# Optimization experiments

Measured on AMD Instinct MI355X. Metric: run time of the kernel, lower is better.

The kernel has to match this reference:

```python
import jax, jax.numpy as jnp
import numpy as np

B, N, S, K = 8, 16384, 1024, 32
C_STEM, C_PATCH, PE_DIM = 64, 128, 24
RADIUS = 0.2
NUM_BANDS = PE_DIM // 6  # 4 freq bands, sin+cos per xyz axis -> 3*2*4 = 24


def setup_inputs() -> dict:
    key = jax.random.key(0)
    ks = jax.random.split(key, 6)
    xyz = jax.random.uniform(ks[0], (B, N, 3), dtype=jnp.float32)
    point_feature = jax.random.normal(ks[1], (B, N, C_STEM), dtype=jnp.float32)
    patch_center = jax.random.uniform(ks[2], (B, S, 3), dtype=jnp.float32)
    in_dim = C_STEM + 3 + PE_DIM  # grouped_feature + relative_xyz + pos-enc
    w1 = jax.random.normal(ks[3], (in_dim, C_PATCH), dtype=jnp.float32) / np.sqrt(in_dim)
    b1 = jnp.zeros((C_PATCH,), dtype=jnp.float32)
    w2 = jax.random.normal(ks[4], (C_PATCH, C_PATCH), dtype=jnp.float32) / np.sqrt(C_PATCH)
    b2 = jnp.zeros((C_PATCH,), dtype=jnp.float32)
    return dict(xyz=xyz, point_feature=point_feature, patch_center=patch_center,
                w1=w1, b1=b1, w2=w2, b2=b2)


def query_ball_point(radius, nsample, xyz, new_xyz):
    # Standard PointNet++ ball query. xyz:[B,N,3], new_xyz:[B,S,3] -> idx:[B,S,K]
    n = xyz.shape[1]
    sqrdists = jnp.sum((new_xyz[:, :, None, :] - xyz[:, None, :, :]) ** 2, axis=-1)  # [B,S,N]
    gi = jnp.where(sqrdists > radius * radius, n,
                   jnp.arange(n, dtype=jnp.int32)[None, None, :])
    gi = jnp.sort(gi, axis=-1)[:, :, :nsample]           # first K in-ball indices
    first = gi[:, :, :1]
    gi = jnp.where(gi == n, first, gi)                   # pad misses with first hit
    return jnp.minimum(gi, n - 1)


def index_points(points, idx):
    # points:[B,N,C], idx:[B,S,K] -> [B,S,K,C]
    b = points.shape[0]
    return points[jnp.arange(b)[:, None, None], idx]


def pos_encode(rel):
    # NeRF-style sinusoidal encoding of relative xyz: [...,3] -> [...,PE_DIM]
    freqs = (2.0 ** jnp.arange(NUM_BANDS, dtype=jnp.float32)) * jnp.pi
    ang = rel[..., None] * freqs                          # [...,3,NB]
    enc = jnp.concatenate([jnp.sin(ang), jnp.cos(ang)], axis=-1)  # [...,3,2NB]
    return enc.reshape(rel.shape[:-1] + (PE_DIM,))


def reference(xyz, point_feature, patch_center, w1, b1, w2, b2):
    neighbor_idx = query_ball_point(RADIUS, K, xyz, patch_center)   # [B,S,K]
    grouped_xyz = index_points(xyz, neighbor_idx)                    # [B,S,K,3]
    grouped_feature = index_points(point_feature, neighbor_idx)      # [B,S,K,C_STEM]
    relative_xyz = grouped_xyz - patch_center[:, :, None, :]
    relative_position = pos_encode(relative_xyz)                     # [B,S,K,PE_DIM]
    grouped_input = jnp.concatenate(
        (grouped_feature, relative_xyz, relative_position), axis=-1)  # [B,S,K,91]
    h = jax.nn.relu(grouped_input @ w1 + b1)   # PointMLP 1 (shared per-point MLP)
    h = h @ w2 + b2                            # PointMLP 2 (no activation)
    patch_feature = jnp.max(h, axis=2)         # max-pool over K neighbors -> [B,S,C_PATCH]
    return (patch_feature, neighbor_idx)
```

## Files before the change

### kernel.cpp

```cpp
#include <hip/hip_runtime.h>
#include <hip/hip_bf16.h>

#define B_ 8
#define N_ 16384
#define S_ 1024
#define K_ 32
#define CSTEM 64
#define CPATCH 128
#define INDIM 91
#define LDH 136

typedef __attribute__((ext_vector_type(8))) short short8v;
typedef __attribute__((ext_vector_type(4))) float f32x4;

static __device__ __forceinline__ unsigned short f2bf(float f) {
  union { float f; unsigned int u; } v; v.f = f;
  return (unsigned short)((v.u + 0x7FFFu + ((v.u >> 16) & 1u)) >> 16);
}

static __device__ __forceinline__ short8v cvt8(const float4 a, const float4 b) {
  unsigned short v[8];
  v[0] = f2bf(a.x); v[1] = f2bf(a.y); v[2] = f2bf(a.z); v[3] = f2bf(a.w);
  v[4] = f2bf(b.x); v[5] = f2bf(b.y); v[6] = f2bf(b.z); v[7] = f2bf(b.w);
  return *(const short8v*)v;
}

static __device__ __forceinline__ short8v pe_frag(
    float r0, float r1, float r2, int kq)
{
  unsigned short v[8];
  #pragma unroll
  for (int j = 0; j < 8; ++j) {
    const int c = 64 + kq + j;
    float val;
    if (c < 67) {
      val = (c == 64) ? r0 : ((c == 65) ? r1 : r2);
    } else if (c < 91) {
      const int qq = c - 67, d = qq >> 3, rbit = qq & 7, band = rbit & 3;
      const float rel = (d == 0) ? r0 : ((d == 1) ? r1 : r2);
      const float ang = rel * ((float)(1 << band) * 3.14159265358979323846f);
      val = (rbit < 4) ? __sinf(ang) : __cosf(ang);
    } else {
      val = 0.f;
    }
    v[j] = f2bf(val);
  }
  return *(const short8v*)v;
}

__global__ __launch_bounds__(256) void pack_weights(
    const float* __restrict__ w1, const float* __restrict__ w2,
    unsigned short* __restrict__ w1p, unsigned short* __restrict__ w2p)
{
  const int id = blockIdx.x * 256 + threadIdx.x;
  if (id < 3 * 8 * 64) {
    const int l = id & 63, ct = (id >> 6) & 7, ks = id >> 9;
    const int col = 16 * ct + (l & 15);
    const int kb = 32 * ks + (l >> 4) * 8;
    unsigned short v[8];
    #pragma unroll
    for (int j = 0; j < 8; ++j) {
      const int k = kb + j;
      v[j] = (k < INDIM) ? f2bf(w1[k * CPATCH + col]) : (unsigned short)0;
    }
    *(short8v*)&w1p[(size_t)id * 8] = *(const short8v*)v;
  } else if (id < 3 * 8 * 64 + 4 * 8 * 64) {
    const int id2 = id - 3 * 8 * 64;
    const int l = id2 & 63, ct = (id2 >> 6) & 7, ks = id2 >> 9;
    const int col = 16 * ct + (l & 15);
    const int kb = 32 * ks + (l >> 4) * 8;
    unsigned short v[8];
    #pragma unroll
    for (int j = 0; j < 8; ++j) v[j] = f2bf(w2[(kb + j) * CPATCH + col]);
    *(short8v*)&w2p[(size_t)id2 * 8] = *(const short8v*)v;
  }
}

#define TEST4(V0, V1, V2, MASKVAR) do {                                    \
    MASKVAR = 0u;                                                          \
    const float X[4] = {(V0).x, (V0).w, (V1).z, (V2).y};                   \
    const float Y[4] = {(V0).y, (V1).x, (V1).w, (V2).z};                   \
    const float Z[4] = {(V0).z, (V1).y, (V2).x, (V2).w};                   \
    _Pragma("unroll")                                                      \
    for (int p = 0; p < 4; ++p) {                                          \
      const float dxf = X[p] - cx, dyf = Y[p] - cy, dzf = Z[p] - cz;       \
      const float d2f = fmaf(dxf, dxf, fmaf(dyf, dyf, dzf * dzf));         \
      bool in;                                                             \
      if (fabsf(d2f - 0.04f) <= 1e-5f) {                                   \
        const double dx = (double)X[p] - (double)cx;                       \
        const double dy = (double)Y[p] - (double)cy;                       \
        const double dz = (double)Z[p] - (double)cz;                       \
        in = (dx * dx + dy * dy + dz * dz) <= (0.2 * 0.2);                 \
      } else {                                                             \
        in = (d2f < 0.04f);                                                \
      }                                                                    \
      if (in) MASKVAR |= (1u << p);                                        \
    }                                                                      \
  } while (0)

#define APPEND4(MASKVAR, POSVAR, I0, V0, V1, V2) do {                      \
    if ((MASKVAR) & 1u) { if ((POSVAR) < K_) { sidx[POSVAR] = (I0) + 0;    \
      sxyz[POSVAR][0] = (V0).x; sxyz[POSVAR][1] = (V0).y;                  \
      sxyz[POSVAR][2] = (V0).z; } ++(POSVAR); }                            \
    if ((MASKVAR) & 2u) { if ((POSVAR) < K_) { sidx[POSVAR] = (I0) + 1;    \
      sxyz[POSVAR][0] = (V0).w; sxyz[POSVAR][1] = (V1).x;                  \
      sxyz[POSVAR][2] = (V1).y; } ++(POSVAR); }                            \
    if ((MASKVAR) & 4u) { if ((POSVAR) < K_) { sidx[POSVAR] = (I0) + 2;    \
      sxyz[POSVAR][0] = (V1).z; sxyz[POSVAR][1] = (V1).w;                  \
      sxyz[POSVAR][2] = (V2).x; } ++(POSVAR); }                            \
    if ((MASKVAR) & 8u) { if ((POSVAR) < K_) { sidx[POSVAR] = (I0) + 3;    \
      sxyz[POSVAR][0] = (V2).y; sxyz[POSVAR][1] = (V2).z;                  \
      sxyz[POSVAR][2] = (V2).w; } ++(POSVAR); }                            \
  } while (0)

__global__ __launch_bounds__(64, 4) void fused_wave(
    const float* __restrict__ xyz, const float* __restrict__ pf,
    const float* __restrict__ pc,
    const unsigned short* __restrict__ w1p, const float* __restrict__ b1,
    const unsigned short* __restrict__ w2p, const float* __restrict__ b2,
    float* __restrict__ idx_out, float* __restrict__ out)
{
  const int lane = threadIdx.x;
  const int bs   = blockIdx.x;
  const int b    = bs >> 10;

  __shared__ int   sidx[K_];
  __shared__ float sxyz[K_][3];
  __shared__ __align__(16) unsigned short Hs[K_][LDH];

  const float* __restrict__ xb  = xyz + (size_t)b * N_ * 3;
  const float* __restrict__ pfb = pf  + (size_t)b * N_ * CSTEM;
  const float cx = pc[bs * 3 + 0];
  const float cy = pc[bs * 3 + 1];
  const float cz = pc[bs * 3 + 2];

  int found = 0;
  {
    const int lo3 = lane * 12;
    int base = 0;
    float4 v0 = *(const float4*)&xb[lo3 + 0];
    float4 v1 = *(const float4*)&xb[lo3 + 4];
    float4 v2 = *(const float4*)&xb[lo3 + 8];
    float4 v3 = *(const float4*)&xb[256 * 3 + lo3 + 0];
    float4 v4 = *(const float4*)&xb[256 * 3 + lo3 + 4];
    float4 v5 = *(const float4*)&xb[256 * 3 + lo3 + 8];

    for (;;) {
      const int nb = (base + 512 < N_) ? base + 512 : base;
      const float4 n0 = *(const float4*)&xb[nb * 3 + lo3 + 0];
      const float4 n1 = *(const float4*)&xb[nb * 3 + lo3 + 4];
      const float4 n2 = *(const float4*)&xb[nb * 3 + lo3 + 8];
      const float4 n3 = *(const float4*)&xb[(nb + 256) * 3 + lo3 + 0];
      const float4 n4 = *(const float4*)&xb[(nb + 256) * 3 + lo3 + 4];
      const float4 n5 = *(const float4*)&xb[(nb + 256) * 3 + lo3 + 8];

      unsigned m0, m1;
      TEST4(v0, v1, v2, m0);
      TEST4(v3, v4, v5, m1);

      const int c0 = __popc(m0), c1 = __popc(m1);
      unsigned incl = (unsigned)c0 | ((unsigned)c1 << 16);
      #pragma unroll
      for (int d = 1; d < 64; d <<= 1) {
        const unsigned t = (unsigned)__shfl_up((int)incl, d);
        if (lane >= d) incl += t;
      }
      const unsigned tot = (unsigned)__shfl((int)incl, 63);
      const int t0 = (int)(tot & 0xFFFFu), t1 = (int)(tot >> 16);

      int pos0 = found + (int)((incl & 0xFFFFu)) - c0;
      int pos1 = found + t0 + (int)(incl >> 16) - c1;
      const int i0 = base + lane * 4;
      APPEND4(m0, pos0, i0, v0, v1, v2);
      APPEND4(m1, pos1, i0 + 256, v3, v4, v5);

      found += t0 + t1;
      if (found >= K_) break;
      base += 512;
      if (base >= N_) break;
      v0 = n0; v1 = n1; v2 = n2; v3 = n3; v4 = n4; v5 = n5;
    }
  }

  if (lane == 0 && found == 0) {
    sidx[0] = N_ - 1;
    sxyz[0][0] = xb[(N_ - 1) * 3 + 0];
    sxyz[0][1] = xb[(N_ - 1) * 3 + 1];
    sxyz[0][2] = xb[(N_ - 1) * 3 + 2];
  }
  __threadfence_block();

  if (lane < K_) {
    const int   fill = sidx[0];
    const float fx = sxyz[0][0];
    const float fy = sxyz[0][1];
    const float fz = sxyz[0][2];
    const int v = (lane < found) ? sidx[lane] : fill;
    if (lane >= found) {
      sidx[lane] = fill;
      sxyz[lane][0] = fx;
      sxyz[lane][1] = fy;
      sxyz[lane][2] = fz;
    }
    idx_out[(size_t)bs * K_ + lane] = (float)v;
  }
  __threadfence_block();

  const int rfr  = lane & 15;
  const int koff = (lane >> 4) * 8;

  const int r0 = sidx[rfr];
  const int r1 = sidx[16 + rfr];
  const float4 u00 = *(const float4*)&pfb[(size_t)r0 * CSTEM + koff];
  const float4 u01 = *(const float4*)&pfb[(size_t)r0 * CSTEM + koff + 4];
  const float4 u02 = *(const float4*)&pfb[(size_t)r0 * CSTEM + 32 + koff];
  const float4 u03 = *(const float4*)&pfb[(size_t)r0 * CSTEM + 32 + koff + 4];
  const float4 u10 = *(const float4*)&pfb[(size_t)r1 * CSTEM + koff];
  const float4 u11 = *(const float4*)&pfb[(size_t)r1 * CSTEM + koff + 4];
  const float4 u12 = *(const float4*)&pfb[(size_t)r1 * CSTEM + 32 + koff];
  const float4 u13 = *(const float4*)&pfb[(size_t)r1 * CSTEM + 32 + koff + 4];

  const short8v a0k2 = pe_frag(sxyz[rfr][0] - cx,
                               sxyz[rfr][1] - cy,
                               sxyz[rfr][2] - cz, koff);
  const short8v a1k2 = pe_frag(sxyz[16 + rfr][0] - cx,
                               sxyz[16 + rfr][1] - cy,
                               sxyz[16 + rfr][2] - cz, koff);
  const short8v a0k0 = cvt8(u00, u01), a0k1 = cvt8(u02, u03);
  const short8v a1k0 = cvt8(u10, u11), a1k1 = cvt8(u12, u13);

  #pragma unroll
  for (int c = 0; c < 4; ++c) {
    const short8v bA0 = *(const short8v*)&w1p[((size_t)(0 * 8 + 2 * c + 0) * 64 + lane) * 8];
    const short8v bA1 = *(const short8v*)&w1p[((size_t)(0 * 8 + 2 * c + 1) * 64 + lane) * 8];
    const short8v bB0 = *(const short8v*)&w1p[((size_t)(1 * 8 + 2 * c + 0) * 64 + lane) * 8];
    const short8v bB1 = *(const short8v*)&w1p[((size_t)(1 * 8 + 2 * c + 1) * 64 + lane) * 8];
    const short8v bC0 = *(const short8v*)&w1p[((size_t)(2 * 8 + 2 * c + 0) * 64 + lane) * 8];
    const short8v bC1 = *(const short8v*)&w1p[((size_t)(2 * 8 + 2 * c + 1) * 64 + lane) * 8];

    f32x4 acc[2][2] = {};
    acc[0][0] = __builtin_amdgcn_mfma_f32_16x16x32_bf16(a0k0, bA0, acc[0][0], 0, 0, 0);
    acc[0][1] = __builtin_amdgcn_mfma_f32_16x16x32_bf16(a0k0, bA1, acc[0][1], 0, 0, 0);
    acc[1][0] = __builtin_amdgcn_mfma_f32_16x16x32_bf16(a1k0, bA0, acc[1][0], 0, 0, 0);
    acc[1][1] = __builtin_amdgcn_mfma_f32_16x16x32_bf16(a1k0, bA1, acc[1][1], 0, 0, 0);
    acc[0][0] = __builtin_amdgcn_mfma_f32_16x16x32_bf16(a0k1, bB0, acc[0][0], 0, 0, 0);
    acc[0][1] = __builtin_amdgcn_mfma_f32_16x16x32_bf16(a0k1, bB1, acc[0][1], 0, 0, 0);
    acc[1][0] = __builtin_amdgcn_mfma_f32_16x16x32_bf16(a1k1, bB0, acc[1][0], 0, 0, 0);
    acc[1][1] = __builtin_amdgcn_mfma_f32_16x16x32_bf16(a1k1, bB1, acc[1][1], 0, 0, 0);
    acc[0][0] = __builtin_amdgcn_mfma_f32_16x16x32_bf16(a0k2, bC0, acc[0][0], 0, 0, 0);
    acc[0][1] = __builtin_amdgcn_mfma_f32_16x16x32_bf16(a0k2, bC1, acc[0][1], 0, 0, 0);
    acc[1][0] = __builtin_amdgcn_mfma_f32_16x16x32_bf16(a1k2, bC0, acc[1][0], 0, 0, 0);
    acc[1][1] = __builtin_amdgcn_mfma_f32_16x16x32_bf16(a1k2, bC1, acc[1][1], 0, 0, 0);

    const float bia0 = b1[32 * c + rfr];
    const float bia1 = b1[32 * c + 16 + rfr];
    #pragma unroll
    for (int rt = 0; rt < 2; ++rt)
      #pragma unroll
      for (int reg = 0; reg < 4; ++reg) {
        const int row = 16 * rt + (lane >> 4) * 4 + reg;
        Hs[row][32 * c + rfr]      = f2bf(fmaxf(acc[rt][0][reg] + bia0, 0.f));
        Hs[row][32 * c + 16 + rfr] = f2bf(fmaxf(acc[rt][1][reg] + bia1, 0.f));
      }
  }

  short8v hf[8];
  #pragma unroll
  for (int ks = 0; ks < 4; ++ks) {
    hf[ks * 2 + 0] = *(const short8v*)&Hs[rfr][ks * 32 + koff];
    hf[ks * 2 + 1] = *(const short8v*)&Hs[16 + rfr][ks * 32 + koff];
  }

  #pragma unroll
  for (int c = 0; c < 4; ++c) {
    f32x4 acc2[2][2] = {};
    #pragma unroll
    for (int ks = 0; ks < 4; ++ks) {
      const short8v b0 = *(const short8v*)&w2p[((size_t)(ks * 8 + 2 * c + 0) * 64 + lane) * 8];
      const short8v b1v = *(const short8v*)&w2p[((size_t)(ks * 8 + 2 * c + 1) * 64 + lane) * 8];
      acc2[0][0] = __builtin_amdgcn_mfma_f32_16x16x32_bf16(hf[ks * 2 + 0], b0,  acc2[0][0], 0, 0, 0);
      acc2[0][1] = __builtin_amdgcn_mfma_f32_16x16x32_bf16(hf[ks * 2 + 0], b1v, acc2[0][1], 0, 0, 0);
      acc2[1][0] = __builtin_amdgcn_mfma_f32_16x16x32_bf16(hf[ks * 2 + 1], b0,  acc2[1][0], 0, 0, 0);
      acc2[1][1] = __builtin_amdgcn_mfma_f32_16x16x32_bf16(hf[ks * 2 + 1], b1v, acc2[1][1], 0, 0, 0);
    }
    float m0 = -3.4e38f, m1 = -3.4e38f;
    #pragma unroll
    for (int rt = 0; rt < 2; ++rt)
      #pragma unroll
      for (int reg = 0; reg < 4; ++reg) {
        m0 = fmaxf(m0, acc2[rt][0][reg]);
        m1 = fmaxf(m1, acc2[rt][1][reg]);
      }
    m0 += b2[32 * c + rfr];
    m1 += b2[32 * c + 16 + rfr];
    m0 = fmaxf(m0, __shfl_xor(m0, 16));
    m0 = fmaxf(m0, __shfl_xor(m0, 32));
    m1 = fmaxf(m1, __shfl_xor(m1, 16));
    m1 = fmaxf(m1, __shfl_xor(m1, 32));
    if (lane < 16) {
      out[(size_t)bs * CPATCH + 32 * c + lane]      = m0;
      out[(size_t)bs * CPATCH + 32 * c + 16 + lane] = m1;
    }
  }
}

extern "C" void kernel_launch(void* const* d_in, const int* in_sizes, int n_in,
                              void* d_out, int out_size, void* d_ws, size_t ws_size,
                              hipStream_t stream) {
  const float* xyz = (const float*)d_in[0];
  const float* pf  = (const float*)d_in[1];
  const float* pc  = (const float*)d_in[2];
  const float* w1  = (const float*)d_in[3];
  const float* b1  = (const float*)d_in[4];
  const float* w2  = (const float*)d_in[5];
  const float* b2  = (const float*)d_in[6];

  float* out     = (float*)d_out;
  float* idx_out = out + (size_t)B_ * S_ * CPATCH;

  unsigned short* w1p = (unsigned short*)d_ws;
  unsigned short* w2p = w1p + 96 * 128;

  pack_weights<<<14, 256, 0, stream>>>(w1, w2, w1p, w2p);
  fused_wave<<<B_ * S_, 64, 0, stream>>>(xyz, pf, pc, w1p, b1, w2p, b2,
                                         idx_out, out);
}
```

Baseline: 46.60 us.

## Hoist fp64 ball-boundary fix out of hot loop and software-pipeline weight loads

The ball-query test now computes an in-mask and a near-boundary band mask in fp32, and runs the fp64 recheck only when some lane in the wave has a band hit. That keeps the double-precision branch out of the common path. The padding pass that rewrote shared sidx/sxyz behind a second fence is removed; consumers select entry 0 for slots beyond `found`. The W1 and W2 fragment loads are double-buffered so the next chunk's weights are fetched while the current MFMAs run, at the cost of more live vector registers.

```diff
diff --git a/kernel.cpp b/kernel.cpp
--- a/kernel.cpp
+++ b/kernel.cpp
@@ -76,8 +76,8 @@
   }
 }
 
-#define TEST4(V0, V1, V2, MASKVAR) do {                                    \
-    MASKVAR = 0u;                                                          \
+#define TEST4FB(V0, V1, V2, MASKVAR, BANDVAR) do {                         \
+    MASKVAR = 0u; BANDVAR = 0u;                                            \
     const float X[4] = {(V0).x, (V0).w, (V1).z, (V2).y};                   \
     const float Y[4] = {(V0).y, (V1).x, (V1).w, (V2).z};                   \
     const float Z[4] = {(V0).z, (V1).y, (V2).x, (V2).w};                   \
@@ -85,16 +85,26 @@
     for (int p = 0; p < 4; ++p) {                                          \
       const float dxf = X[p] - cx, dyf = Y[p] - cy, dzf = Z[p] - cz;       \
       const float d2f = fmaf(dxf, dxf, fmaf(dyf, dyf, dzf * dzf));         \
-      bool in;                                                             \
-      if (fabsf(d2f - 0.04f) <= 1e-5f) {                                   \
-        const double dx = (double)X[p] - (double)cx;                       \
-        const double dy = (double)Y[p] - (double)cy;                       \
-        const double dz = (double)Z[p] - (double)cz;                       \
-        in = (dx * dx + dy * dy + dz * dz) <= (0.2 * 0.2);                 \
-      } else {                                                             \
-        in = (d2f < 0.04f);                                                \
+      if (fabsf(d2f - 0.04f) <= 1e-5f) BANDVAR |= (1u << p);               \
+      if (d2f < 0.04f) MASKVAR |= (1u << p);                               \
+    }                                                                      \
+  } while (0)
+
+#define FIX4(BANDVAR, MASKVAR, V0, V1, V2) do {                            \
+    if (BANDVAR) {                                                         \
+      const float X[4] = {(V0).x, (V0).w, (V1).z, (V2).y};                 \
+      const float Y[4] = {(V0).y, (V1).x, (V1).w, (V2).z};                 \
+      const float Z[4] = {(V0).z, (V1).y, (V2).x, (V2).w};                 \
+      _Pragma("unroll")                                                    \
+      for (int p = 0; p < 4; ++p) {                                        \
+        if ((BANDVAR >> p) & 1u) {                                         \
+          const double dx = (double)X[p] - (double)cx;                     \
+          const double dy = (double)Y[p] - (double)cy;                     \
+          const double dz = (double)Z[p] - (double)cz;                     \
+          const bool in64 = (dx * dx + dy * dy + dz * dz) <= (0.2 * 0.2);  \
+          MASKVAR = (MASKVAR & ~(1u << p)) | ((unsigned)in64 << p);        \
+        }                                                                  \
       }                                                                    \
-      if (in) MASKVAR |= (1u << p);                                        \
     }                                                                      \
   } while (0)
 
@@ -113,6 +123,11 @@
       sxyz[POSVAR][2] = (V2).w; } ++(POSVAR); }                            \
   } while (0)
 
+#define LDW1(KS, C, T) \
+  (*(const short8v*)&w1p[((size_t)((KS) * 8 + 2 * (C) + (T)) * 64 + lane) * 8])
+#define LDW2(KS, C, T) \
+  (*(const short8v*)&w2p[((size_t)((KS) * 8 + 2 * (C) + (T)) * 64 + lane) * 8])
+
 __global__ __launch_bounds__(64, 4) void fused_wave(
     const float* __restrict__ xyz, const float* __restrict__ pf,
     const float* __restrict__ pc,
@@ -154,9 +169,13 @@
       const float4 n4 = *(const float4*)&xb[(nb + 256) * 3 + lo3 + 4];
       const float4 n5 = *(const float4*)&xb[(nb + 256) * 3 + lo3 + 8];
 
-      unsigned m0, m1;
-      TEST4(v0, v1, v2, m0);
-      TEST4(v3, v4, v5, m1);
+      unsigned m0, m1, bd0, bd1;
+      TEST4FB(v0, v1, v2, m0, bd0);
+      TEST4FB(v3, v4, v5, m1, bd1);
+      if (__any((int)(bd0 | bd1))) {
+        FIX4(bd0, m0, v0, v1, v2);
+        FIX4(bd1, m1, v3, v4, v5);
+      }
 
       const int c0 = __popc(m0), c1 = __popc(m1);
       unsigned incl = (unsigned)c0 | ((unsigned)c1 << 16);
@@ -168,7 +187,7 @@
       const unsigned tot = (unsigned)__shfl((int)incl, 63);
       const int t0 = (int)(tot & 0xFFFFu), t1 = (int)(tot >> 16);
 
-      int pos0 = found + (int)((incl & 0xFFFFu)) - c0;
+      int pos0 = found + (int)(incl & 0xFFFFu) - c0;
       int pos1 = found + t0 + (int)(incl >> 16) - c1;
       const int i0 = base + lane * 4;
       APPEND4(m0, pos0, i0, v0, v1, v2);
@@ -190,27 +209,12 @@
   }
   __threadfence_block();
 
-  if (lane < K_) {
-    const int   fill = sidx[0];
-    const float fx = sxyz[0][0];
-    const float fy = sxyz[0][1];
-    const float fz = sxyz[0][2];
-    const int v = (lane < found) ? sidx[lane] : fill;
-    if (lane >= found) {
-      sidx[lane] = fill;
-      sxyz[lane][0] = fx;
-      sxyz[lane][1] = fy;
-      sxyz[lane][2] = fz;
-    }
-    idx_out[(size_t)bs * K_ + lane] = (float)v;
-  }
-  __threadfence_block();
-
   const int rfr  = lane & 15;
   const int koff = (lane >> 4) * 8;
 
-  const int r0 = sidx[rfr];
-  const int r1 = sidx[16 + rfr];
+  const int r0 = (rfr < found)      ? sidx[rfr]      : sidx[0];
+  const int r1 = (16 + rfr < found) ? sidx[16 + rfr] : sidx[0];
+
   const float4 u00 = *(const float4*)&pfb[(size_t)r0 * CSTEM + koff];
   const float4 u01 = *(const float4*)&pfb[(size_t)r0 * CSTEM + koff + 4];
   const float4 u02 = *(const float4*)&pfb[(size_t)r0 * CSTEM + 32 + koff];
@@ -220,49 +224,66 @@
   const float4 u12 = *(const float4*)&pfb[(size_t)r1 * CSTEM + 32 + koff];
   const float4 u13 = *(const float4*)&pfb[(size_t)r1 * CSTEM + 32 + koff + 4];
 
-  const short8v a0k2 = pe_frag(sxyz[rfr][0] - cx,
-                               sxyz[rfr][1] - cy,
-                               sxyz[rfr][2] - cz, koff);
-  const short8v a1k2 = pe_frag(sxyz[16 + rfr][0] - cx,
-                               sxyz[16 + rfr][1] - cy,
-                               sxyz[16 + rfr][2] - cz, koff);
+  if (lane < K_) {
+    const int vout = (lane < found) ? sidx[lane] : sidx[0];
+    idx_out[(size_t)bs * K_ + lane] = (float)vout;
+  }
+
+  const float sxa = (rfr < found) ? sxyz[rfr][0] : sxyz[0][0];
+  const float sya = (rfr < found) ? sxyz[rfr][1] : sxyz[0][1];
+  const float sza = (rfr < found) ? sxyz[rfr][2] : sxyz[0][2];
+  const float sxb2 = (16 + rfr < found) ? sxyz[16 + rfr][0] : sxyz[0][0];
+  const float syb2 = (16 + rfr < found) ? sxyz[16 + rfr][1] : sxyz[0][1];
+  const float szb2 = (16 + rfr < found) ? sxyz[16 + rfr][2] : sxyz[0][2];
+
+  const short8v a0k2 = pe_frag(sxa - cx, sya - cy, sza - cz, koff);
+  const short8v a1k2 = pe_frag(sxb2 - cx, syb2 - cy, szb2 - cz, koff);
   const short8v a0k0 = cvt8(u00, u01), a0k1 = cvt8(u02, u03);
   const short8v a1k0 = cvt8(u10, u11), a1k1 = cvt8(u12, u13);
 
-  #pragma unroll
-  for (int c = 0; c < 4; ++c) {
-    const short8v bA0 = *(const short8v*)&w1p[((size_t)(0 * 8 + 2 * c + 0) * 64 + lane) * 8];
-    const short8v bA1 = *(const short8v*)&w1p[((size_t)(0 * 8 + 2 * c + 1) * 64 + lane) * 8];
-    const short8v bB0 = *(const short8v*)&w1p[((size_t)(1 * 8 + 2 * c + 0) * 64 + lane) * 8];
-    const short8v bB1 = *(const short8v*)&w1p[((size_t)(1 * 8 + 2 * c + 1) * 64 + lane) * 8];
-    const short8v bC0 = *(const short8v*)&w1p[((size_t)(2 * 8 + 2 * c + 0) * 64 + lane) * 8];
-    const short8v bC1 = *(const short8v*)&w1p[((size_t)(2 * 8 + 2 * c + 1) * 64 + lane) * 8];
-
-    f32x4 acc[2][2] = {};
-    acc[0][0] = __builtin_amdgcn_mfma_f32_16x16x32_bf16(a0k0, bA0, acc[0][0], 0, 0, 0);
-    acc[0][1] = __builtin_amdgcn_mfma_f32_16x16x32_bf16(a0k0, bA1, acc[0][1], 0, 0, 0);
-    acc[1][0] = __builtin_amdgcn_mfma_f32_16x16x32_bf16(a1k0, bA0, acc[1][0], 0, 0, 0);
-    acc[1][1] = __builtin_amdgcn_mfma_f32_16x16x32_bf16(a1k0, bA1, acc[1][1], 0, 0, 0);
-    acc[0][0] = __builtin_amdgcn_mfma_f32_16x16x32_bf16(a0k1, bB0, acc[0][0], 0, 0, 0);
-    acc[0][1] = __builtin_amdgcn_mfma_f32_16x16x32_bf16(a0k1, bB1, acc[0][1], 0, 0, 0);
-    acc[1][0] = __builtin_amdgcn_mfma_f32_16x16x32_bf16(a1k1, bB0, acc[1][0], 0, 0, 0);
-    acc[1][1] = __builtin_amdgcn_mfma_f32_16x16x32_bf16(a1k1, bB1, acc[1][1], 0, 0, 0);
-    acc[0][0] = __builtin_amdgcn_mfma_f32_16x16x32_bf16(a0k2, bC0, acc[0][0], 0, 0, 0);
-    acc[0][1] = __builtin_amdgcn_mfma_f32_16x16x32_bf16(a0k2, bC1, acc[0][1], 0, 0, 0);
-    acc[1][0] = __builtin_amdgcn_mfma_f32_16x16x32_bf16(a1k2, bC0, acc[1][0], 0, 0, 0);
-    acc[1][1] = __builtin_amdgcn_mfma_f32_16x16x32_bf16(a1k2, bC1, acc[1][1], 0, 0, 0);
-
-    const float bia0 = b1[32 * c + rfr];
-    const float bia1 = b1[32 * c + 16 + rfr];
-    #pragma unroll
-    for (int rt = 0; rt < 2; ++rt)
-      #pragma unroll
-      for (int reg = 0; reg < 4; ++reg) {
-        const int row = 16 * rt + (lane >> 4) * 4 + reg;
-        Hs[row][32 * c + rfr]      = f2bf(fmaxf(acc[rt][0][reg] + bia0, 0.f));
-        Hs[row][32 * c + 16 + rfr] = f2bf(fmaxf(acc[rt][1][reg] + bia1, 0.f));
-      }
-  }
+  short8v wA0, wA1, wB0, wB1, wC0, wC1;
+  short8v xA0, xA1, xB0, xB1, xC0, xC1;
+  wA0 = LDW1(0, 0, 0); wA1 = LDW1(0, 0, 1);
+  wB0 = LDW1(1, 0, 0); wB1 = LDW1(1, 0, 1);
+  wC0 = LDW1(2, 0, 0); wC1 = LDW1(2, 0, 1);
+
+#define L1_CHUNK(C, A0,A1,B0,B1,C0,C1, P0,P1,P2,P3,P4,P5, PREF)            \
+  do {                                                                     \
+    if (PREF) {                                                            \
+      P0 = LDW1(0, (C) + 1, 0); P1 = LDW1(0, (C) + 1, 1);                  \
+      P2 = LDW1(1, (C) + 1, 0); P3 = LDW1(1, (C) + 1, 1);                  \
+      P4 = LDW1(2, (C) + 1, 0); P5 = LDW1(2, (C) + 1, 1);                  \
+    }                                                                      \
+    f32x4 acc[2][2] = {};                                                  \
+    acc[0][0] = __builtin_amdgcn_mfma_f32_16x16x32_bf16(a0k0, A0, acc[0][0], 0, 0, 0); \
+    acc[0][1] = __builtin_amdgcn_mfma_f32_16x16x32_bf16(a0k0, A1, acc[0][1], 0, 0, 0); \
+    acc[1][0] = __builtin_amdgcn_mfma_f32_16x16x32_bf16(a1k0, A0, acc[1][0], 0, 0, 0); \
+    acc[1][1] = __builtin_amdgcn_mfma_f32_16x16x32_bf16(a1k0, A1, acc[1][1], 0, 0, 0); \
+    acc[0][0] = __builtin_amdgcn_mfma_f32_16x16x32_bf16(a0k1, B0, acc[0][0], 0, 0, 0); \
+    acc[0][1] = __builtin_amdgcn_mfma_f32_16x16x32_bf16(a0k1, B1, acc[0][1], 0, 0, 0); \
+    acc[1][0] = __builtin_amdgcn_mfma_f32_16x16x32_bf16(a1k1, B0, acc[1][0], 0, 0, 0); \
+    acc[1][1] = __builtin_amdgcn_mfma_f32_16x16x32_bf16(a1k1, B1, acc[1][1], 0, 0, 0); \
+    acc[0][0] = __builtin_amdgcn_mfma_f32_16x16x32_bf16(a0k2, C0, acc[0][0], 0, 0, 0); \
+    acc[0][1] = __builtin_amdgcn_mfma_f32_16x16x32_bf16(a0k2, C1, acc[0][1], 0, 0, 0); \
+    acc[1][0] = __builtin_amdgcn_mfma_f32_16x16x32_bf16(a1k2, C0, acc[1][0], 0, 0, 0); \
+    acc[1][1] = __builtin_amdgcn_mfma_f32_16x16x32_bf16(a1k2, C1, acc[1][1], 0, 0, 0); \
+    const float bia0 = b1[32 * (C) + rfr];                                 \
+    const float bia1 = b1[32 * (C) + 16 + rfr];                            \
+    _Pragma("unroll")                                                      \
+    for (int rt = 0; rt < 2; ++rt)                                         \
+      _Pragma("unroll")                                                    \
+      for (int reg = 0; reg < 4; ++reg) {                                  \
+        const int row = 16 * rt + (lane >> 4) * 4 + reg;                   \
+        Hs[row][32 * (C) + rfr]      = f2bf(fmaxf(acc[rt][0][reg] + bia0, 0.f)); \
+        Hs[row][32 * (C) + 16 + rfr] = f2bf(fmaxf(acc[rt][1][reg] + bia1, 0.f)); \
+      }                                                                    \
+  } while (0)
+
+  L1_CHUNK(0, wA0,wA1,wB0,wB1,wC0,wC1, xA0,xA1,xB0,xB1,xC0,xC1, true);
+  L1_CHUNK(1, xA0,xA1,xB0,xB1,xC0,xC1, wA0,wA1,wB0,wB1,wC0,wC1, true);
+  L1_CHUNK(2, wA0,wA1,wB0,wB1,wC0,wC1, xA0,xA1,xB0,xB1,xC0,xC1, true);
+  L1_CHUNK(3, xA0,xA1,xB0,xB1,xC0,xC1, wA0,wA1,wB0,wB1,wC0,wC1, false);
+#undef L1_CHUNK
 
   short8v hf[8];
   #pragma unroll
@@ -271,18 +292,26 @@
     hf[ks * 2 + 1] = *(const short8v*)&Hs[16 + rfr][ks * 32 + koff];
   }
 
+  short8v p0 = LDW2(0, 0, 0), p1 = LDW2(0, 0, 1);
+  short8v q0, q1;
+
+#define L2_STEP(KS, CUR0, CUR1, NXT0, NXT1, NC, NKS, LAST)                 \
+  do {                                                                     \
+    if (!(LAST)) { NXT0 = LDW2(NKS, NC, 0); NXT1 = LDW2(NKS, NC, 1); }     \
+    acc2[0][0] = __builtin_amdgcn_mfma_f32_16x16x32_bf16(hf[(KS) * 2 + 0], CUR0, acc2[0][0], 0, 0, 0); \
+    acc2[0][1] = __builtin_amdgcn_mfma_f32_16x16x32_bf16(hf[(KS) * 2 + 0], CUR1, acc2[0][1], 0, 0, 0); \
+    acc2[1][0] = __builtin_amdgcn_mfma_f32_16x16x32_bf16(hf[(KS) * 2 + 1], CUR0, acc2[1][0], 0, 0, 0); \
+    acc2[1][1] = __builtin_amdgcn_mfma_f32_16x16x32_bf16(hf[(KS) * 2 + 1], CUR1, acc2[1][1], 0, 0, 0); \
+  } while (0)
+
   #pragma unroll
   for (int c = 0; c < 4; ++c) {
     f32x4 acc2[2][2] = {};
-    #pragma unroll
-    for (int ks = 0; ks < 4; ++ks) {
-      const short8v b0 = *(const short8v*)&w2p[((size_t)(ks * 8 + 2 * c + 0) * 64 + lane) * 8];
-      const short8v b1v = *(const short8v*)&w2p[((size_t)(ks * 8 + 2 * c + 1) * 64 + lane) * 8];
-      acc2[0][0] = __builtin_amdgcn_mfma_f32_16x16x32_bf16(hf[ks * 2 + 0], b0,  acc2[0][0], 0, 0, 0);
-      acc2[0][1] = __builtin_amdgcn_mfma_f32_16x16x32_bf16(hf[ks * 2 + 0], b1v, acc2[0][1], 0, 0, 0);
-      acc2[1][0] = __builtin_amdgcn_mfma_f32_16x16x32_bf16(hf[ks * 2 + 1], b0,  acc2[1][0], 0, 0, 0);
-      acc2[1][1] = __builtin_amdgcn_mfma_f32_16x16x32_bf16(hf[ks * 2 + 1], b1v, acc2[1][1], 0, 0, 0);
-    }
+    L2_STEP(0, p0, p1, q0, q1, c, 1, false);
+    L2_STEP(1, q0, q1, p0, p1, c, 2, false);
+    L2_STEP(2, p0, p1, q0, q1, c, 3, false);
+    L2_STEP(3, q0, q1, p0, p1, c + 1, 0, c == 3);
+
     float m0 = -3.4e38f, m1 = -3.4e38f;
     #pragma unroll
     for (int rt = 0; rt < 2; ++rt)
@@ -302,6 +331,7 @@
       out[(size_t)bs * CPATCH + 32 * c + 16 + lane] = m1;
     }
   }
+#undef L2_STEP
 }
 
 extern "C" void kernel_launch(void* const* d_in, const int* in_sizes, int n_in,
```

Result: no change. 45.83 us (-1.7%).
